# Optimization experiments

Hardware: AMD Instinct MI355X
Metric: run time of the kernel (lower is better)

## Reference

```python
import jax, jax.numpy as jnp
import numpy as np

B, T, D_IN, D_OUT = 4, 2048, 1024, 1024


def setup_inputs() -> dict:
    key = jax.random.key(0)
    k1, k2, k3, k4 = jax.random.split(key, 4)
    s_in = 1.0 / np.sqrt(D_IN)
    return {
        "input_vector": jax.random.normal(k1, (B, T, D_IN), dtype=jnp.float32),
        "w_q": jax.random.normal(k2, (D_IN, D_OUT), dtype=jnp.float32) * s_in,
        "w_k": jax.random.normal(k3, (D_IN, D_OUT), dtype=jnp.float32) * s_in,
        "w_v": jax.random.normal(k4, (D_IN, D_OUT), dtype=jnp.float32) * s_in,
    }


def reference(input_vector, w_q, w_k, w_v):
    # projections: [B, T, D_OUT]
    q = jnp.einsum("btd,de->bte", input_vector, w_q)
    k = jnp.einsum("btd,de->bte", input_vector, w_k)
    v = jnp.einsum("btd,de->bte", input_vector, w_v)

    T_ = q.shape[1]
    # raw scores [B, T, T]
    scores = jnp.einsum("bqd,bkd->bqk", q, k)
    # causal mask (strict upper triangle masked to -inf), applied BEFORE scaling
    # (as in the original; -inf is invariant under the scale anyway)
    causal = jnp.tril(jnp.ones((T_, T_), dtype=bool))  # True = keep
    scores = jnp.where(causal[None, :, :], scores, -jnp.inf)
    scores = scores / jnp.sqrt(jnp.asarray(k.shape[-1], scores.dtype))
    attn = jax.nn.softmax(scores, axis=-1)
    # dropout = 0.0 (eval): identity
    return jnp.einsum("bqk,bkd->bqd", attn, v)
```

## Files before the change

kernel.cpp:

```cpp
#include <hip/hip_runtime.h>
#include <cstdint>

typedef unsigned short u16;
typedef __attribute__((ext_vector_type(8))) short short8;
typedef __attribute__((ext_vector_type(16))) float f32x16;

__device__ __forceinline__ u16 f2bf(float f) {
  uint32_t u = __float_as_uint(f);
  u += 0x7FFFu + ((u >> 16) & 1u);
  return (u16)(u >> 16);
}

__device__ __forceinline__ void async_ld16(u16* lds, const u16* g) {
  __builtin_amdgcn_global_load_lds((const __attribute__((address_space(1))) uint32_t*)g,
                                   (__attribute__((address_space(3))) uint32_t*)lds,
                                   16, 0, 0);
}

template <int ROLE>
__global__ __launch_bounds__(256) void gk(
    const u16* __restrict__ Xbf, const u16* __restrict__ Wt,
    u16* __restrict__ QK, u16* __restrict__ VtAll,
    u16* __restrict__ P, float* __restrict__ lpart,
    float* __restrict__ out)
{
  const int b = blockIdx.x;
  const int tid = threadIdx.x;
  const int lane = tid & 63;
  const int wave = tid >> 6;
  const int wr = (wave >> 1) * 64;
  const int wc = (wave & 1) * 64;

  __shared__ __align__(16) u16 ls[4][4096];
  __shared__ float l_s[128];

  const int c0 = tid, c1 = tid + 256;
  const int r0 = c0 >> 2, q0 = ((c0 & 3) ^ ((c0 >> 3) & 3)) * 8;
  const int r1 = c1 >> 2, q1 = ((c1 & 3) ^ ((c1 >> 3) & 3)) * 8;

  const int m32 = lane & 31;
  const int hh = lane >> 5;
  const int rsw = (m32 >> 1) & 3;
  int offA[2][2], offB[2][2];
#pragma unroll
  for (int i = 0; i < 2; ++i)
#pragma unroll
    for (int ks = 0; ks < 2; ++ks) {
      const int kq = ((ks << 1) | hh) ^ rsw;
      offA[i][ks] = (wr + i * 32 + m32) * 32 + kq * 8;
      offB[i][ks] = (wc + i * 32 + m32) * 32 + kq * 8;
    }

  const u16 *A, *B;
  int lda, ldb, kmax, m0, n0, mb, nb, zb = 0, mat = 0;
  bool scoresRole = false;

  if constexpr (ROLE == 0) {
    const int u = b & 7, v = b >> 3;
    mat = v >> 6;
    const int w = v & 63;
    nb = w & 7;
    mb = u * 8 + (w >> 3);
    A = Xbf; lda = 1024;
    B = Wt + (long)mat * 1024 * 1024; ldb = 1024;
    kmax = 1024;
  } else if constexpr (ROLE == 1) {
    if (b < 544) {
      scoresRole = true;
      const int u = b & 7, t = b >> 3;
      zb = t / 17;
      const int idx = t % 17;
      if (idx <= u) { mb = u;      nb = idx; }
      else          { mb = 15 - u; nb = idx - u - 1; }
      A = QK + (long)zb * 2048 * 1024; lda = 1024;
      B = QK + 8192L * 1024 + (long)zb * 2048 * 1024; ldb = 1024;
      kmax = 1024;
    } else {
      const int v = b - 544;
      const int u = v & 7, w = v >> 3;
      mb = w & 7;
      nb = u * 8 + (w >> 3);
      A = Wt + 2L * 1024 * 1024; lda = 1024;
      B = Xbf; ldb = 1024;
      kmax = 1024;
    }
  } else {
    const int u = b & 7, idx = b >> 3;
    zb = blockIdx.y;
    if (idx < 8) { mb = 15 - u; nb = idx; }
    else         { mb = u;      nb = idx - 8; }
    A = P + (long)zb * 2048 * 2048; lda = 2048;
    B = VtAll + (long)zb * 2048; ldb = 8192;
    kmax = (mb + 1) * 128;
  }
  m0 = mb * 128;
  n0 = nb * 128;

  const u16* pA0 = A + (long)(m0 + r0) * lda + q0;
  const u16* pA1 = A + (long)(m0 + r1) * lda + q1;
  const u16* pB0 = B + (long)(n0 + r0) * ldb + q0;
  const u16* pB1 = B + (long)(n0 + r1) * ldb + q1;

  f32x16 acc[2][2];
#pragma unroll
  for (int i = 0; i < 2; ++i)
#pragma unroll
    for (int j = 0; j < 2; ++j)
#pragma unroll
      for (int r = 0; r < 16; ++r) acc[i][j][r] = 0.f;

  async_ld16(&ls[0][c0 * 8 - 0], pA0);
  async_ld16(&ls[0][c1 * 8 - 2048 * 0], pA1);
  async_ld16(&ls[2][c0 * 8], pB0);
  async_ld16(&ls[2][c1 * 8 - 2048 * 0], pB1);
  pA0 += 32; pA1 += 32; pB0 += 32; pB1 += 32;

  int p = 0;
  for (int k0 = 0; k0 < kmax; k0 += 32) {
    __syncthreads();
    if (k0 + 32 < kmax) {
      u16* la = ls[p ^ 1];
      u16* lb = ls[2 + (p ^ 1)];
      async_ld16(&la[c0 * 8], pA0);
      async_ld16(&la[c1 * 8], pA1);
      async_ld16(&lb[c0 * 8], pB0);
      async_ld16(&lb[c1 * 8], pB1);
      pA0 += 32; pA1 += 32; pB0 += 32; pB1 += 32;
    }

    const u16* la = ls[p];
    const u16* lb = ls[2 + p];
#pragma unroll
    for (int ks = 0; ks < 2; ++ks) {
      const short8 a0 = *(const short8*)&la[offA[0][ks]];
      const short8 a1 = *(const short8*)&la[offA[1][ks]];
      const short8 b0 = *(const short8*)&lb[offB[0][ks]];
      const short8 b1 = *(const short8*)&lb[offB[1][ks]];
      acc[0][0] = __builtin_amdgcn_mfma_f32_32x32x16_bf16(a0, b0, acc[0][0], 0, 0, 0);
      acc[0][1] = __builtin_amdgcn_mfma_f32_32x32x16_bf16(a0, b1, acc[0][1], 0, 0, 0);
      acc[1][0] = __builtin_amdgcn_mfma_f32_32x32x16_bf16(a1, b0, acc[1][0], 0, 0, 0);
      acc[1][1] = __builtin_amdgcn_mfma_f32_32x32x16_bf16(a1, b1, acc[1][1], 0, 0, 0);
    }
    p ^= 1;
  }

  const int ec = lane & 31;
  const int rb = (lane >> 5) * 4;

  if constexpr (ROLE == 0) {
    u16* C = QK + (long)mat * 8192 * 1024;
#pragma unroll
    for (int i = 0; i < 2; ++i) {
      const int rbase = m0 + wr + i * 32 + rb;
#pragma unroll
      for (int j = 0; j < 2; ++j) {
        const int col = n0 + wc + j * 32 + ec;
#pragma unroll
        for (int r = 0; r < 16; ++r) {
          const int row = rbase + (r & 3) + 8 * (r >> 2);
          C[(long)row * 1024 + col] = f2bf(acc[i][j][r]);
        }
      }
    }
  } else if constexpr (ROLE == 1) {
    if (scoresRole) {
      u16* C = P + (long)zb * 2048 * 2048;
      float* lp = lpart + (long)zb * 32 * 2048 + (long)(2 * nb + (wc >> 6)) * 2048;
#pragma unroll
      for (int i = 0; i < 2; ++i) {
        const int rbl = wr + i * 32 + rb;
        float rsum[16];
#pragma unroll
        for (int r = 0; r < 16; ++r) rsum[r] = 0.f;
#pragma unroll
        for (int j = 0; j < 2; ++j) {
          const int col = n0 + wc + j * 32 + ec;
#pragma unroll
          for (int r = 0; r < 16; ++r) {
            const int row = m0 + rbl + (r & 3) + 8 * (r >> 2);
            float pv = __expf(acc[i][j][r] * 0.03125f);
            if (col > row) pv = 0.f;
            C[(long)row * 2048 + col] = f2bf(pv);
            rsum[r] += pv;
          }
        }
#pragma unroll
        for (int r = 0; r < 16; ++r) {
          float s = rsum[r];
#pragma unroll
          for (int off = 1; off < 32; off <<= 1) s += __shfl_xor(s, off, 64);
          if ((lane & 31) == 0)
            lp[m0 + rbl + (r & 3) + 8 * (r >> 2)] = s;
        }
      }
    } else {
#pragma unroll
      for (int i = 0; i < 2; ++i) {
        const int rbase = m0 + wr + i * 32 + rb;
#pragma unroll
        for (int j = 0; j < 2; ++j) {
          const int col = n0 + wc + j * 32 + ec;
#pragma unroll
          for (int r = 0; r < 16; ++r) {
            const int row = rbase + (r & 3) + 8 * (r >> 2);
            VtAll[(long)row * 8192 + col] = f2bf(acc[i][j][r]);
          }
        }
      }
    }
  } else {
    __syncthreads();
    if (tid < 128) {
      const float* lp = lpart + (long)zb * 32 * 2048 + m0 + tid;
      float s0 = 0.f, s1 = 0.f;
      const int nch = 2 * (mb + 1);
      for (int c = 0; c < nch; c += 2) {
        s0 += lp[(long)c * 2048];
        s1 += lp[(long)(c + 1) * 2048];
      }
      l_s[tid] = 1.f / (s0 + s1);
    }
    __syncthreads();
    float* C = out + (long)zb * 2048 * 1024;
#pragma unroll
    for (int i = 0; i < 2; ++i) {
      const int rbl = wr + i * 32 + rb;
#pragma unroll
      for (int j = 0; j < 2; ++j) {
        const int col = n0 + wc + j * 32 + ec;
#pragma unroll
        for (int r = 0; r < 16; ++r) {
          const int rl = rbl + (r & 3) + 8 * (r >> 2);
          C[(long)(m0 + rl) * 1024 + col] = acc[i][j][r] * l_s[rl];
        }
      }
    }
  }
}

__global__ __launch_bounds__(256) void cast_fused(
    const float* __restrict__ x, const float* __restrict__ w0,
    const float* __restrict__ w1, const float* __restrict__ w2,
    u16* __restrict__ Xbf, u16* __restrict__ Wt)
{
  const int b = blockIdx.x;
  if (b < 8192) {
    const long i = ((long)b * 256 + threadIdx.x) * 4;
    const float4 v = *(const float4*)(x + i);
    ushort4 o;
    o.x = f2bf(v.x); o.y = f2bf(v.y); o.z = f2bf(v.z); o.w = f2bf(v.w);
    *(ushort4*)(Xbf + i) = o;
  } else {
    const int bb = b - 8192;
    const int z = bb >> 10, rem = bb & 1023;
    const float* W = (z == 0) ? w0 : (z == 1) ? w1 : w2;
    u16* o = Wt + (long)z * 1024 * 1024;
    __shared__ float t[32][33];
    const int n0 = (rem & 31) * 32, k0 = (rem >> 5) * 32;
    const int tx = threadIdx.x & 31, ty = threadIdx.x >> 5;
    for (int r = ty; r < 32; r += 8) t[r][tx] = W[(long)(k0 + r) * 1024 + n0 + tx];
    __syncthreads();
    for (int r = ty; r < 32; r += 8) o[(long)(n0 + r) * 1024 + k0 + tx] = f2bf(t[tx][r]);
  }
}

extern "C" void kernel_launch(void* const* d_in, const int* in_sizes, int n_in,
                              void* d_out, int out_size, void* d_ws, size_t ws_size,
                              hipStream_t stream) {
  const float* X  = (const float*)d_in[0];
  const float* Wq = (const float*)d_in[1];
  const float* Wk = (const float*)d_in[2];
  const float* Wv = (const float*)d_in[3];
  float* out = (float*)d_out;

  u16* Xbf   = (u16*)d_ws;
  u16* Wt    = Xbf + 8192L * 1024;
  u16* QK    = Wt + 3L * 1024 * 1024;
  u16* VtAll = QK + 2L * 8192 * 1024;
  u16* P     = VtAll + 1024L * 8192;
  float* lpart = (float*)(P + 4L * 2048 * 2048);

  cast_fused<<<8192 + 3072, 256, 0, stream>>>(X, Wq, Wk, Wv, Xbf, Wt);

  gk<0><<<1024, 256, 0, stream>>>(Xbf, Wt, QK, VtAll, P, lpart, out);

  gk<1><<<1056, 256, 0, stream>>>(Xbf, Wt, QK, VtAll, P, lpart, out);

  gk<2><<<dim3(128, 4), 256, 0, stream>>>(Xbf, Wt, QK, VtAll, P, lpart, out);
}
```

Measured before the change: 248.6 us.

## Replace projection and score GEMMs with 256x256-tile 8-wave ping-pong kernel

Adds a new g8 kernel with 256x256 output tiles, 512 threads, a 64-wide K step and a hand-scheduled ping-pong pipeline. The pipeline interleaves LDS reads, async global-to-LDS staging, explicit waitcnt fences, barriers and MFMA priority boosts. The Q/K/V projections and the causal score tiles now run in this kernel, and V^T moves into the first launch so the second launch only computes scores. The aim is more data reuse per tile and better overlap of loads with MFMA. The cost is coarser causal tiles: more wasted work above the diagonal and fewer blocks, which can hurt load balance.

```diff
diff --git a/kernel.cpp b/kernel.cpp
--- a/kernel.cpp
+++ b/kernel.cpp
@@ -15,6 +15,228 @@
   __builtin_amdgcn_global_load_lds((const __attribute__((address_space(1))) uint32_t*)g,
                                    (__attribute__((address_space(3))) uint32_t*)lds,
                                    16, 0, 0);
+}
+
+__device__ __forceinline__ void lgkm0_fence() {
+  asm volatile("s_waitcnt lgkmcnt(0)" ::: "memory");
+  __builtin_amdgcn_sched_barrier(0);
+}
+__device__ __forceinline__ void vmw6_fence() {
+  asm volatile("s_waitcnt vmcnt(6)" ::: "memory");
+  __builtin_amdgcn_sched_barrier(0);
+}
+__device__ __forceinline__ void vmw0_fence() {
+  asm volatile("s_waitcnt vmcnt(0)" ::: "memory");
+  __builtin_amdgcn_sched_barrier(0);
+}
+
+#define MFMA32 __builtin_amdgcn_mfma_f32_32x32x16_bf16
+
+template <int ROLE>
+__global__ __launch_bounds__(512, 2) void g8(
+    const u16* __restrict__ Xbf, const u16* __restrict__ Wt,
+    u16* __restrict__ QK, u16* __restrict__ VtAll,
+    u16* __restrict__ P, float* __restrict__ lpart)
+{
+  const int b = blockIdx.x;
+  const int tid = threadIdx.x;
+  const int lane = tid & 63;
+  const int wave = tid >> 6;
+  const int wr2 = wave >> 2;
+  const int wc2 = wave & 3;
+  const int m32 = lane & 31;
+  const int hh = lane >> 5;
+
+  __shared__ __align__(16) u16 ls[2][2][16384];
+
+  const u16 *A, *B;
+  u16* C = nullptr;
+  long ldc = 1024;
+  int m0, n0, zb = 0, nt = 0;
+
+  if constexpr (ROLE == 0) {
+    if (b < 256) {
+      const int mat = b >> 7, v = b & 127;
+      m0 = (v >> 2) * 256;
+      n0 = (v & 3) * 256;
+      A = Xbf;
+      B = Wt + (long)mat * 1024 * 1024;
+      C = QK + (long)mat * 8192 * 1024;
+      ldc = 1024;
+    } else {
+      const int v = b - 256;
+      m0 = (v >> 5) * 256;
+      n0 = (v & 31) * 256;
+      A = Wt + 2L * 1024 * 1024;
+      B = Xbf;
+      C = VtAll;
+      ldc = 8192;
+    }
+  } else {
+    zb = b / 36;
+    const int w = b - zb * 36;
+    int mt = 0;
+    while ((mt + 1) * (mt + 2) / 2 <= w) ++mt;
+    nt = w - mt * (mt + 1) / 2;
+    m0 = mt * 256;
+    n0 = nt * 256;
+    A = QK + (long)zb * 2048 * 1024;
+    B = QK + 8192L * 1024 + (long)zb * 2048 * 1024;
+  }
+
+  const int sr = tid >> 3, sg = tid & 7;
+  const u16* pAst = A + (long)(m0 + sr) * 1024 + ((sg ^ (sr & 7)) * 8);
+  const u16* pBst = B + (long)(n0 + sr) * 1024 + ((sg ^ (sr & 7)) * 8);
+
+#define STG_A(bf, h, t_) do { \
+    u16* _d = &ls[bf][0][(h) * 8192] + tid * 8; \
+    const u16* _s = pAst + (long)(h) * 131072 + (long)(t_) * 64; \
+    async_ld16(_d, _s); async_ld16(_d + 4096, _s + 65536); } while (0)
+#define STG_B(bf, h, t_) do { \
+    u16* _d = &ls[bf][1][(h) * 8192] + tid * 8; \
+    const u16* _s = pBst + (long)(h) * 131072 + (long)(t_) * 64; \
+    async_ld16(_d, _s); async_ld16(_d + 4096, _s + 65536); } while (0)
+
+  int offAk[4], offBk[4];
+#pragma unroll
+  for (int ks = 0; ks < 4; ++ks) {
+    const int kq = ((ks << 1) | hh) ^ (m32 & 7);
+    offAk[ks] = (wr2 * 128 + m32) * 64 + kq * 8;
+    offBk[ks] = (wc2 * 64 + m32) * 64 + kq * 8;
+  }
+
+  f32x16 acc[4][2];
+#pragma unroll
+  for (int i = 0; i < 4; ++i)
+#pragma unroll
+    for (int j = 0; j < 2; ++j)
+#pragma unroll
+      for (int r = 0; r < 16; ++r) acc[i][j][r] = 0.f;
+
+  STG_A(0, 0, 0); STG_A(0, 1, 0); STG_B(0, 0, 0); STG_B(0, 1, 0);
+  STG_B(1, 0, 1); STG_B(1, 1, 1); STG_A(1, 0, 1);
+  vmw6_fence();
+  __builtin_amdgcn_s_barrier();
+
+  short8 A0[4], A1[4], A2[4], A3[4], B0r[4], B1r[4];
+
+#pragma unroll 1
+  for (int t = 0; t < 16; ++t) {
+    const u16* la = ls[t & 1][0];
+    const u16* lb = ls[t & 1][1];
+
+#pragma unroll
+    for (int ks = 0; ks < 4; ++ks) {
+      A0[ks]  = *(const short8*)&la[offAk[ks]];
+      A1[ks]  = *(const short8*)&la[offAk[ks] + 2048];
+      B0r[ks] = *(const short8*)&lb[offBk[ks]];
+    }
+    if (t < 15) STG_A((t + 1) & 1, 1, t + 1);
+    __builtin_amdgcn_s_barrier();
+    lgkm0_fence();
+    __builtin_amdgcn_s_setprio(1);
+#pragma unroll
+    for (int ks = 0; ks < 4; ++ks) {
+      acc[0][0] = MFMA32(A0[ks], B0r[ks], acc[0][0], 0, 0, 0);
+      acc[1][0] = MFMA32(A1[ks], B0r[ks], acc[1][0], 0, 0, 0);
+    }
+    __builtin_amdgcn_s_setprio(0);
+    __builtin_amdgcn_s_barrier();
+
+#pragma unroll
+    for (int ks = 0; ks < 4; ++ks)
+      B1r[ks] = *(const short8*)&lb[offBk[ks] + 2048];
+    __builtin_amdgcn_s_barrier();
+    lgkm0_fence();
+    __builtin_amdgcn_s_setprio(1);
+#pragma unroll
+    for (int ks = 0; ks < 4; ++ks) {
+      acc[0][1] = MFMA32(A0[ks], B1r[ks], acc[0][1], 0, 0, 0);
+      acc[1][1] = MFMA32(A1[ks], B1r[ks], acc[1][1], 0, 0, 0);
+    }
+    __builtin_amdgcn_s_setprio(0);
+    __builtin_amdgcn_s_barrier();
+
+#pragma unroll
+    for (int ks = 0; ks < 4; ++ks) {
+      A2[ks] = *(const short8*)&la[offAk[ks] + 4096];
+      A3[ks] = *(const short8*)&la[offAk[ks] + 6144];
+    }
+    if (t < 14) STG_B(t & 1, 0, t + 2);
+    __builtin_amdgcn_s_barrier();
+    lgkm0_fence();
+    __builtin_amdgcn_s_setprio(1);
+#pragma unroll
+    for (int ks = 0; ks < 4; ++ks) {
+      acc[2][0] = MFMA32(A2[ks], B0r[ks], acc[2][0], 0, 0, 0);
+      acc[3][0] = MFMA32(A3[ks], B0r[ks], acc[3][0], 0, 0, 0);
+    }
+    __builtin_amdgcn_s_setprio(0);
+    __builtin_amdgcn_s_barrier();
+
+    if (t < 14) { STG_B(t & 1, 1, t + 2); STG_A(t & 1, 0, t + 2); }
+    __builtin_amdgcn_s_barrier();
+    __builtin_amdgcn_s_setprio(1);
+#pragma unroll
+    for (int ks = 0; ks < 4; ++ks) {
+      acc[2][1] = MFMA32(A2[ks], B1r[ks], acc[2][1], 0, 0, 0);
+      acc[3][1] = MFMA32(A3[ks], B1r[ks], acc[3][1], 0, 0, 0);
+    }
+    __builtin_amdgcn_s_setprio(0);
+    if (t < 14) vmw6_fence(); else vmw0_fence();
+    __builtin_amdgcn_s_barrier();
+  }
+#undef STG_A
+#undef STG_B
+
+  const int ec = lane & 31;
+  const int rb = hh * 4;
+
+  if constexpr (ROLE == 0) {
+#pragma unroll
+    for (int i = 0; i < 4; ++i) {
+      const int rbase = m0 + wr2 * 128 + i * 32 + rb;
+#pragma unroll
+      for (int j = 0; j < 2; ++j) {
+        const int col = n0 + wc2 * 64 + j * 32 + ec;
+#pragma unroll
+        for (int r = 0; r < 16; ++r) {
+          const int row = rbase + (r & 3) + 8 * (r >> 2);
+          C[(long)row * ldc + col] = f2bf(acc[i][j][r]);
+        }
+      }
+    }
+  } else {
+    u16* Cp = P + (long)zb * 2048 * 2048;
+    float* lp = lpart + (long)zb * 32 * 2048 + (long)(nt * 4 + wc2) * 2048;
+#pragma unroll
+    for (int i = 0; i < 4; ++i) {
+      const int rbl = wr2 * 128 + i * 32 + rb;
+      float rsum[16];
+#pragma unroll
+      for (int r = 0; r < 16; ++r) rsum[r] = 0.f;
+#pragma unroll
+      for (int j = 0; j < 2; ++j) {
+        const int col = n0 + wc2 * 64 + j * 32 + ec;
+#pragma unroll
+        for (int r = 0; r < 16; ++r) {
+          const int row = m0 + rbl + (r & 3) + 8 * (r >> 2);
+          float pv = __expf(acc[i][j][r] * 0.03125f);
+          if (col > row) pv = 0.f;
+          Cp[(long)row * 2048 + col] = f2bf(pv);
+          rsum[r] += pv;
+        }
+      }
+#pragma unroll
+      for (int r = 0; r < 16; ++r) {
+        float s = rsum[r];
+#pragma unroll
+        for (int off = 1; off < 32; off <<= 1) s += __shfl_xor(s, off, 64);
+        if ((lane & 31) == 0)
+          lp[m0 + rbl + (r & 3) + 8 * (r >> 2)] = s;
+      }
+    }
+  }
 }
 
 template <int ROLE>
@@ -52,47 +274,14 @@
     }
 
   const u16 *A, *B;
-  int lda, ldb, kmax, m0, n0, mb, nb, zb = 0, mat = 0;
-  bool scoresRole = false;
-
-  if constexpr (ROLE == 0) {
-    const int u = b & 7, v = b >> 3;
-    mat = v >> 6;
-    const int w = v & 63;
-    nb = w & 7;
-    mb = u * 8 + (w >> 3);
-    A = Xbf; lda = 1024;
-    B = Wt + (long)mat * 1024 * 1024; ldb = 1024;
-    kmax = 1024;
-  } else if constexpr (ROLE == 1) {
-    if (b < 544) {
-      scoresRole = true;
-      const int u = b & 7, t = b >> 3;
-      zb = t / 17;
-      const int idx = t % 17;
-      if (idx <= u) { mb = u;      nb = idx; }
-      else          { mb = 15 - u; nb = idx - u - 1; }
-      A = QK + (long)zb * 2048 * 1024; lda = 1024;
-      B = QK + 8192L * 1024 + (long)zb * 2048 * 1024; ldb = 1024;
-      kmax = 1024;
-    } else {
-      const int v = b - 544;
-      const int u = v & 7, w = v >> 3;
-      mb = w & 7;
-      nb = u * 8 + (w >> 3);
-      A = Wt + 2L * 1024 * 1024; lda = 1024;
-      B = Xbf; ldb = 1024;
-      kmax = 1024;
-    }
-  } else {
-    const int u = b & 7, idx = b >> 3;
-    zb = blockIdx.y;
-    if (idx < 8) { mb = 15 - u; nb = idx; }
-    else         { mb = u;      nb = idx - 8; }
-    A = P + (long)zb * 2048 * 2048; lda = 2048;
-    B = VtAll + (long)zb * 2048; ldb = 8192;
-    kmax = (mb + 1) * 128;
-  }
+  int lda, ldb, kmax, m0, n0, mb, nb, zb = 0;
+  const int u = b & 7, idx = b >> 3;
+  zb = blockIdx.y;
+  if (idx < 8) { mb = 15 - u; nb = idx; }
+  else         { mb = u;      nb = idx - 8; }
+  A = P + (long)zb * 2048 * 2048; lda = 2048;
+  B = VtAll + (long)zb * 2048; ldb = 8192;
+  kmax = (mb + 1) * 128;
   m0 = mb * 128;
   n0 = nb * 128;
 
@@ -109,10 +298,10 @@
 #pragma unroll
       for (int r = 0; r < 16; ++r) acc[i][j][r] = 0.f;
 
-  async_ld16(&ls[0][c0 * 8 - 0], pA0);
-  async_ld16(&ls[0][c1 * 8 - 2048 * 0], pA1);
+  async_ld16(&ls[0][c0 * 8], pA0);
+  async_ld16(&ls[0][c1 * 8], pA1);
   async_ld16(&ls[2][c0 * 8], pB0);
-  async_ld16(&ls[2][c1 * 8 - 2048 * 0], pB1);
+  async_ld16(&ls[2][c1 * 8], pB1);
   pA0 += 32; pA1 += 32; pB0 += 32; pB1 += 32;
 
   int p = 0;
@@ -136,10 +325,10 @@
       const short8 a1 = *(const short8*)&la[offA[1][ks]];
       const short8 b0 = *(const short8*)&lb[offB[0][ks]];
       const short8 b1 = *(const short8*)&lb[offB[1][ks]];
-      acc[0][0] = __builtin_amdgcn_mfma_f32_32x32x16_bf16(a0, b0, acc[0][0], 0, 0, 0);
-      acc[0][1] = __builtin_amdgcn_mfma_f32_32x32x16_bf16(a0, b1, acc[0][1], 0, 0, 0);
-      acc[1][0] = __builtin_amdgcn_mfma_f32_32x32x16_bf16(a1, b0, acc[1][0], 0, 0, 0);
-      acc[1][1] = __builtin_amdgcn_mfma_f32_32x32x16_bf16(a1, b1, acc[1][1], 0, 0, 0);
+      acc[0][0] = MFMA32(a0, b0, acc[0][0], 0, 0, 0);
+      acc[0][1] = MFMA32(a0, b1, acc[0][1], 0, 0, 0);
+      acc[1][0] = MFMA32(a1, b0, acc[1][0], 0, 0, 0);
+      acc[1][1] = MFMA32(a1, b1, acc[1][1], 0, 0, 0);
     }
     p ^= 1;
   }
@@ -147,92 +336,29 @@
   const int ec = lane & 31;
   const int rb = (lane >> 5) * 4;
 
-  if constexpr (ROLE == 0) {
-    u16* C = QK + (long)mat * 8192 * 1024;
-#pragma unroll
-    for (int i = 0; i < 2; ++i) {
-      const int rbase = m0 + wr + i * 32 + rb;
-#pragma unroll
-      for (int j = 0; j < 2; ++j) {
-        const int col = n0 + wc + j * 32 + ec;
-#pragma unroll
-        for (int r = 0; r < 16; ++r) {
-          const int row = rbase + (r & 3) + 8 * (r >> 2);
-          C[(long)row * 1024 + col] = f2bf(acc[i][j][r]);
-        }
-      }
-    }
-  } else if constexpr (ROLE == 1) {
-    if (scoresRole) {
-      u16* C = P + (long)zb * 2048 * 2048;
-      float* lp = lpart + (long)zb * 32 * 2048 + (long)(2 * nb + (wc >> 6)) * 2048;
-#pragma unroll
-      for (int i = 0; i < 2; ++i) {
-        const int rbl = wr + i * 32 + rb;
-        float rsum[16];
-#pragma unroll
-        for (int r = 0; r < 16; ++r) rsum[r] = 0.f;
-#pragma unroll
-        for (int j = 0; j < 2; ++j) {
-          const int col = n0 + wc + j * 32 + ec;
-#pragma unroll
-          for (int r = 0; r < 16; ++r) {
-            const int row = m0 + rbl + (r & 3) + 8 * (r >> 2);
-            float pv = __expf(acc[i][j][r] * 0.03125f);
-            if (col > row) pv = 0.f;
-            C[(long)row * 2048 + col] = f2bf(pv);
-            rsum[r] += pv;
-          }
-        }
-#pragma unroll
-        for (int r = 0; r < 16; ++r) {
-          float s = rsum[r];
-#pragma unroll
-          for (int off = 1; off < 32; off <<= 1) s += __shfl_xor(s, off, 64);
-          if ((lane & 31) == 0)
-            lp[m0 + rbl + (r & 3) + 8 * (r >> 2)] = s;
-        }
-      }
-    } else {
-#pragma unroll
-      for (int i = 0; i < 2; ++i) {
-        const int rbase = m0 + wr + i * 32 + rb;
-#pragma unroll
-        for (int j = 0; j < 2; ++j) {
-          const int col = n0 + wc + j * 32 + ec;
-#pragma unroll
-          for (int r = 0; r < 16; ++r) {
-            const int row = rbase + (r & 3) + 8 * (r >> 2);
-            VtAll[(long)row * 8192 + col] = f2bf(acc[i][j][r]);
-          }
-        }
-      }
-    }
-  } else {
-    __syncthreads();
-    if (tid < 128) {
-      const float* lp = lpart + (long)zb * 32 * 2048 + m0 + tid;
-      float s0 = 0.f, s1 = 0.f;
-      const int nch = 2 * (mb + 1);
-      for (int c = 0; c < nch; c += 2) {
-        s0 += lp[(long)c * 2048];
-        s1 += lp[(long)(c + 1) * 2048];
-      }
-      l_s[tid] = 1.f / (s0 + s1);
-    }
-    __syncthreads();
-    float* C = out + (long)zb * 2048 * 1024;
-#pragma unroll
-    for (int i = 0; i < 2; ++i) {
-      const int rbl = wr + i * 32 + rb;
-#pragma unroll
-      for (int j = 0; j < 2; ++j) {
-        const int col = n0 + wc + j * 32 + ec;
-#pragma unroll
-        for (int r = 0; r < 16; ++r) {
-          const int rl = rbl + (r & 3) + 8 * (r >> 2);
-          C[(long)(m0 + rl) * 1024 + col] = acc[i][j][r] * l_s[rl];
-        }
+  __syncthreads();
+  if (tid < 128) {
+    const float* lp = lpart + (long)zb * 32 * 2048 + m0 + tid;
+    float s0 = 0.f, s1 = 0.f;
+    const int nch = 2 * (mb + 1);
+    for (int c = 0; c < nch; c += 2) {
+      s0 += lp[(long)c * 2048];
+      s1 += lp[(long)(c + 1) * 2048];
+    }
+    l_s[tid] = 1.f / (s0 + s1);
+  }
+  __syncthreads();
+  float* Cf = out + (long)zb * 2048 * 1024;
+#pragma unroll
+  for (int i = 0; i < 2; ++i) {
+    const int rbl = wr + i * 32 + rb;
+#pragma unroll
+    for (int j = 0; j < 2; ++j) {
+      const int col = n0 + wc + j * 32 + ec;
+#pragma unroll
+      for (int r = 0; r < 16; ++r) {
+        const int rl = rbl + (r & 3) + 8 * (r >> 2);
+        Cf[(long)(m0 + rl) * 1024 + col] = acc[i][j][r] * l_s[rl];
       }
     }
   }
@@ -282,9 +408,9 @@
 
   cast_fused<<<8192 + 3072, 256, 0, stream>>>(X, Wq, Wk, Wv, Xbf, Wt);
 
-  gk<0><<<1024, 256, 0, stream>>>(Xbf, Wt, QK, VtAll, P, lpart, out);
-
-  gk<1><<<1056, 256, 0, stream>>>(Xbf, Wt, QK, VtAll, P, lpart, out);
+  g8<0><<<384, 512, 0, stream>>>(Xbf, Wt, QK, VtAll, P, lpart);
+
+  g8<1><<<144, 512, 0, stream>>>(Xbf, Wt, QK, VtAll, P, lpart);
 
   gk<2><<<dim3(128, 4), 256, 0, stream>>>(Xbf, Wt, QK, VtAll, P, lpart, out);
 }
```

Result: slower. 255.3 us (+2.7%).
